# Kernel optimization log

Hardware: AMD Instinct MI355X
Metric: run time of the kernel (lower is better)

Reference implementation:

```python
import jax, jax.numpy as jnp
import numpy as np

D_NODE = 100
D_HID = 300
EPS = 1e-5


def _gru_step_h0(x, W_ih, b_ih, b_hh):
    # Single torch-GRU step with h0 = 0 (seq len 1), so W_hh @ h0 vanishes
    # and only the hidden biases b_hh survive.
    gi = x @ W_ih.T + b_ih                      # [..., 3*H]
    H = D_HID
    r = jax.nn.sigmoid(gi[..., 0:H] + b_hh[0:H])
    z = jax.nn.sigmoid(gi[..., H:2 * H] + b_hh[H:2 * H])
    n = jnp.tanh(gi[..., 2 * H:3 * H] + r * b_hh[2 * H:3 * H])
    return (1.0 - z) * n                        # h' = (1-z)*n + z*0


def setup_inputs() -> dict:
    key = jax.random.key(0)
    ks = jax.random.split(key, 20)
    B, T, Lq, N = 128, 512, 256, 256
    s = 0.02
    inp = {
        "nodes": jax.random.normal(ks[0], (B * N, D_NODE), jnp.float32),
        "context_rep": jax.random.normal(ks[1], (B, Lq, D_HID), jnp.float32),
        "dia_triples": jax.random.randint(ks[2], (B, T, 3), 0, N, jnp.int64 if jax.config.jax_enable_x64 else jnp.int32),
        "node_number": N,
        # mean_trans: Linear(100, 300)
        "W_mean": s * jax.random.normal(ks[3], (D_HID, D_NODE), jnp.float32),
        "b_mean": jnp.zeros((D_HID,), jnp.float32),
        # bidirectional GRU(300 -> 300); h0=0 so W_hh drops out, keep biases
        "W_ih_f": s * jax.random.normal(ks[4], (3 * D_HID, D_HID), jnp.float32),
        "b_ih_f": s * jax.random.normal(ks[5], (3 * D_HID,), jnp.float32),
        "b_hh_f": s * jax.random.normal(ks[6], (3 * D_HID,), jnp.float32),
        "W_ih_b": s * jax.random.normal(ks[7], (3 * D_HID, D_HID), jnp.float32),
        "b_ih_b": s * jax.random.normal(ks[8], (3 * D_HID,), jnp.float32),
        "b_hh_b": s * jax.random.normal(ks[9], (3 * D_HID,), jnp.float32),
        # output_trans: Linear(600, 300) + tanh
        "W_out": s * jax.random.normal(ks[10], (D_HID, 2 * D_HID), jnp.float32),
        "b_out": jnp.zeros((D_HID,), jnp.float32),
        # trans_node_to_decoder_dim: Linear(100, 300)
        "W_node": s * jax.random.normal(ks[11], (D_HID, D_NODE), jnp.float32),
        "b_node": jnp.zeros((D_HID,), jnp.float32),
        # layernorm(300)
        "gamma": jnp.ones((D_HID,), jnp.float32),
        "beta": jnp.zeros((D_HID,), jnp.float32),
    }
    return inp


def reference(nodes, context_rep, dia_triples, node_number,
              W_mean, b_mean, W_ih_f, b_ih_f, b_hh_f,
              W_ih_b, b_ih_b, b_hh_b, W_out, b_out,
              W_node, b_node, gamma, beta):
    B = context_rep.shape[0]
    N = node_number
    T = dia_triples.shape[1]
    nodes3 = nodes.reshape(B, N, D_NODE)                        # per-dialogue node slices

    # gather head/tail nodes of each triple, mean-aggregate
    head = jnp.broadcast_to(dia_triples[:, :, 0][:, :, None], (B, T, D_NODE))
    tail = jnp.broadcast_to(dia_triples[:, :, -1][:, :, None], (B, T, D_NODE))
    gh = jnp.take_along_axis(nodes3, head, axis=1)              # [B,T,100]
    gt = jnp.take_along_axis(nodes3, tail, axis=1)
    tri_mean = 0.5 * (gh + gt)

    x = tri_mean @ W_mean.T + b_mean                            # [B,T,300] GRU inputs (len-1 paths)

    # bidirectional GRU, one step each direction from h0=0
    h_f = _gru_step_h0(x, W_ih_f, b_ih_f, b_hh_f)
    h_b = _gru_step_h0(x, W_ih_b, b_ih_b, b_hh_b)
    hidden = jnp.concatenate([h_f, h_b], axis=-1)               # [B,T,600]

    hid_ = jnp.tanh(hidden @ W_out.T + b_out)                   # [B,T,300]

    # attention: alpha = softmax(query @ hidden^T, -1).sum(0)
    scores = jnp.einsum("bld,btd->blt", context_rep, hid_)
    alpha = jax.nn.softmax(scores, axis=-1).sum(axis=1)         # [B,T]
    rep = jnp.einsum("bt,btd->bd", alpha, hid_)                 # [B,300]

    mu = rep.mean(axis=-1, keepdims=True)
    var = rep.var(axis=-1, keepdims=True)
    path_feature = (rep - mu) * jax.lax.rsqrt(var + EPS) * gamma + beta
    # dropout is identity in eval mode

    node_feature = nodes3 @ W_node.T + b_node                   # [B,N,300]
    node_mask = jnp.zeros((B, 1, N), dtype=bool)                # equal lengths -> no padding
    return path_feature, node_feature, node_mask
```

## Files before the change

### kernel.cpp

```cpp
#include <hip/hip_runtime.h>
#include <math.h>

#define D_NODE 100
#define D_HID  300
static const int TSEQ = 512, LQn = 256, NNODE = 256;

typedef unsigned int u32;
typedef unsigned short u16;
typedef __attribute__((ext_vector_type(8))) short bf16x8;
typedef __attribute__((ext_vector_type(4))) float f32x4;

__device__ __forceinline__ float bflo(u32 u){ return __uint_as_float(u << 16); }
__device__ __forceinline__ float bfhi(u32 u){ return __uint_as_float(u & 0xffff0000u); }
__device__ __forceinline__ float bf2f(u16 v){ return __uint_as_float(((u32)v) << 16); }
__device__ __forceinline__ u16 f2bf(float f){
    u32 u = __float_as_uint(f);
    return (u16)((u + 0x7fffu + ((u >> 16) & 1u)) >> 16);
}
__device__ __forceinline__ u32 pack_bf(float lo, float hi){
    return ((u32)f2bf(lo)) | (((u32)f2bf(hi)) << 16);
}
__device__ __forceinline__ void gload_lds16(const void* g, void* l){
    __builtin_amdgcn_global_load_lds(
        (const __attribute__((address_space(1))) u32*)g,
        (__attribute__((address_space(3))) u32*)l, 16, 0, 0);
}
__device__ __forceinline__ float fsig(float x){
    return __builtin_amdgcn_rcpf(1.f + __expf(-x));
}
__device__ __forceinline__ float ftanh(float x){
    return 1.f - 2.f*__builtin_amdgcn_rcpf(1.f + __expf(2.f*x));
}

__global__ __launch_bounds__(128)
void k0_prep(const float* __restrict__ Wm, const float* __restrict__ bm,
             const float* __restrict__ Wihf, const float* __restrict__ bihf, const float* __restrict__ bhhf,
             const float* __restrict__ Wihb, const float* __restrict__ bihb, const float* __restrict__ bhhb,
             u16* __restrict__ W4bf, float* __restrict__ bc, float* __restrict__ bhhn)
{
    int j = blockIdx.x, g = blockIdx.y, dir = blockIdx.z;
    int tid = threadIdx.x;
    u16* wout = W4bf + ((size_t)((dir*3+g)*320 + j))*128;
    if (j >= D_HID) {
        wout[tid] = 0;
        if (tid == 0) { bc[(dir*3+g)*320 + j] = 0.f; if (g==2) bhhn[dir*320+j] = 0.f; }
        return;
    }
    const float* Wih = dir ? Wihb : Wihf;
    const float* bih = dir ? bihb : bihf;
    const float* bhh = dir ? bhhb : bhhf;
    const float* wrow = Wih + (size_t)(g*D_HID + j)*D_HID;
    int k = tid;
    float s = 0.f;
    if (k < D_NODE)
        for (int q = 0; q < D_HID; ++q)
            s = fmaf(wrow[q], Wm[q*D_NODE + k], s);
    wout[k] = f2bf(k < D_NODE ? s : 0.f);

    __shared__ float red[128];
    float p = 0.f;
    for (int q = tid; q < D_HID; q += 128) p = fmaf(bm[q], wrow[q], p);
    red[tid] = p;
    __syncthreads();
    for (int off = 64; off > 0; off >>= 1) {
        if (tid < off) red[tid] += red[tid + off];
        __syncthreads();
    }
    if (tid == 0) {
        float base = bih[g*D_HID + j] + red[0];
        if (g < 2) base += bhh[g*D_HID + j];
        bc[(dir*3+g)*320 + j] = base;
        if (g == 2) bhhn[dir*320 + j] = bhh[2*D_HID + j];
    }
}

__global__ __launch_bounds__(256)
void kW(const float* __restrict__ Wout, const float* __restrict__ Wnode,
        u16* __restrict__ Woutbf, u16* __restrict__ Wnbf)
{
    int idx = blockIdx.x*256 + threadIdx.x;
    if (idx < 384*608) {
        int j = idx / 608, k = idx % 608;
        float v = (j < D_HID && k < 600) ? Wout[(size_t)j*600 + k] : 0.f;
        Woutbf[idx] = f2bf(v);
    } else {
        int i2 = idx - 384*608;
        if (i2 < 320*128) {
            int j = i2 >> 7, k = i2 & 127;
            float v = (j < D_HID && k < D_NODE) ? Wnode[(size_t)j*D_NODE + k] : 0.f;
            Wnbf[i2] = f2bf(v);
        }
    }
}

__global__ __launch_bounds__(256)
void kA(const float* __restrict__ nodes, const int* __restrict__ trip,
        u32* __restrict__ Abf, u32* __restrict__ Nbf)
{
    int gid = blockIdx.x*256 + threadIdx.x;
    if (gid < 65536) {
        int b = gid >> 9;
        int hidx = trip[(size_t)gid*3];
        int tidx = trip[(size_t)gid*3 + 2];
        const float4* nh = (const float4*)(nodes + ((size_t)b*NNODE + hidx)*D_NODE);
        const float4* nt = (const float4*)(nodes + ((size_t)b*NNODE + tidx)*D_NODE);
        u32* ar = Abf + (size_t)gid*64;
        #pragma unroll 5
        for (int i = 0; i < 25; ++i) {
            float4 a = nh[i], c = nt[i];
            ar[i*2]   = pack_bf(0.5f*(a.x+c.x), 0.5f*(a.y+c.y));
            ar[i*2+1] = pack_bf(0.5f*(a.z+c.z), 0.5f*(a.w+c.w));
        }
        #pragma unroll
        for (int i = 50; i < 64; ++i) ar[i] = 0;
    } else {
        int r = gid - 65536;
        if (r < 32768) {
            const float4* nr = (const float4*)(nodes + (size_t)r*D_NODE);
            u32* ar = Nbf + (size_t)r*64;
            #pragma unroll 5
            for (int i = 0; i < 25; ++i) {
                float4 a = nr[i];
                ar[i*2]   = pack_bf(a.x, a.y);
                ar[i*2+1] = pack_bf(a.z, a.w);
            }
            #pragma unroll
            for (int i = 50; i < 64; ++i) ar[i] = 0;
        }
    }
}

__global__ __launch_bounds__(256)
void kC(const float* __restrict__ ctx, u32* __restrict__ Cbf)
{
    int idx = blockIdx.x*256 + threadIdx.x;
    int r = idx / 160, cp = idx % 160;
    int col = cp*2;
    u32 v = 0;
    if (col < D_HID) {
        float2 f = *(const float2*)(ctx + (size_t)r*D_HID + col);
        v = pack_bf(f.x, f.y);
    }
    Cbf[(size_t)r*160 + cp] = v;
}

__global__ __launch_bounds__(256)
void k1_gru(const u16* __restrict__ Abf, const u16* __restrict__ W4bf,
            const float* __restrict__ bc, const float* __restrict__ bhhn,
            u16* __restrict__ H)
{
    __shared__ char smem[16384];
    int tid = threadIdx.x;
    int lane = tid & 63, w = tid >> 6;
    int l15 = lane & 15, lq = lane >> 4;
    int m0 = blockIdx.x * 64;
    int dir = blockIdx.y / 5;
    int jg = blockIdx.y % 5;
    int j0w = jg*64 + w*16;

    bf16x8 bfr[3][4];
    const u16* Wb = W4bf + (size_t)dir*3*320*128;
    #pragma unroll
    for (int g = 0; g < 3; ++g)
        #pragma unroll
        for (int ks = 0; ks < 4; ++ks)
            bfr[g][ks] = *(const bf16x8*)(Wb + ((size_t)(g*320 + j0w + l15))*128 + ks*32 + lq*8);

    #pragma unroll
    for (int ks = 0; ks < 4; ++ks) {
        const u16* g = Abf + ((size_t)(m0 + w*16 + l15))*128 + ks*32 + lq*8;
        gload_lds16(g, smem + (size_t)((w*4 + ks)*64)*16);
    }
    __syncthreads();

    f32x4 acc[4][3];
    #pragma unroll
    for (int ms = 0; ms < 4; ++ms)
        #pragma unroll
        for (int g = 0; g < 3; ++g)
            acc[ms][g] = (f32x4){0.f,0.f,0.f,0.f};

    #pragma unroll
    for (int ms = 0; ms < 4; ++ms)
        #pragma unroll
        for (int ks = 0; ks < 4; ++ks) {
            bf16x8 a = *(const bf16x8*)(smem + (size_t)(((ms*4+ks)*64 + lane))*16);
            acc[ms][0] = __builtin_amdgcn_mfma_f32_16x16x32_bf16(a, bfr[0][ks], acc[ms][0], 0,0,0);
            acc[ms][1] = __builtin_amdgcn_mfma_f32_16x16x32_bf16(a, bfr[1][ks], acc[ms][1], 0,0,0);
            acc[ms][2] = __builtin_amdgcn_mfma_f32_16x16x32_bf16(a, bfr[2][ks], acc[ms][2], 0,0,0);
        }

    int j = j0w + l15;
    float bcr = bc[(dir*3+0)*320 + j];
    float bcz = bc[(dir*3+1)*320 + j];
    float bcn = bc[(dir*3+2)*320 + j];
    float bn2 = bhhn[dir*320 + j];
    bool ok = (j < D_HID);
    #pragma unroll
    for (int ms = 0; ms < 4; ++ms)
        #pragma unroll
        for (int i = 0; i < 4; ++i) {
            float r = fsig(acc[ms][0][i] + bcr);
            float z = fsig(acc[ms][1][i] + bcz);
            float n = ftanh(acc[ms][2][i] + bcn + r*bn2);
            float h = (1.f - z)*n;
            if (ok) H[(size_t)(m0 + ms*16 + lq*4 + i)*608 + dir*D_HID + j] = f2bf(h);
        }
}

__global__ __launch_bounds__(256, 2)
void k2_out(const u16* __restrict__ H, const u16* __restrict__ Woutbf,
            const float* __restrict__ bout, u16* __restrict__ Hid)
{
    __shared__ char smem[40960];
    int tid = threadIdx.x;
    int lane = tid & 63, w = tid >> 6;
    int l15 = lane & 15, lq = lane >> 4;
    int m0 = blockIdx.x * 64;
    int j0 = blockIdx.y * 128;
    int jA = j0 + w*16, jB = j0 + 64 + w*16;

    bf16x8 bA[19], bB[19];
    #pragma unroll
    for (int ks = 0; ks < 19; ++ks) {
        bA[ks] = *(const bf16x8*)(Woutbf + ((size_t)(jA + l15))*608 + ks*32 + lq*8);
        bB[ks] = *(const bf16x8*)(Woutbf + ((size_t)(jB + l15))*608 + ks*32 + lq*8);
    }
    f32x4 acc[4][2];
    #pragma unroll
    for (int ms = 0; ms < 4; ++ms) { acc[ms][0] = (f32x4){0,0,0,0}; acc[ms][1] = (f32x4){0,0,0,0}; }

    #pragma unroll
    for (int c = 0; c < 2; ++c) {
        const int kb = c ? 10 : 0;
        const int nks = c ? 9 : 10;
        #pragma unroll
        for (int kk = 0; kk < 10; ++kk)
            if (kk < nks) {
                const u16* g = H + ((size_t)(m0 + w*16 + l15))*608 + (kb+kk)*32 + lq*8;
                gload_lds16(g, smem + (size_t)((w*10 + kk)*64)*16);
            }
        __syncthreads();
        #pragma unroll
        for (int ms = 0; ms < 4; ++ms)
            #pragma unroll
            for (int kk = 0; kk < 10; ++kk)
                if (kk < nks) {
                    bf16x8 a = *(const bf16x8*)(smem + (size_t)(((ms*10+kk)*64 + lane))*16);
                    acc[ms][0] = __builtin_amdgcn_mfma_f32_16x16x32_bf16(a, bA[kb+kk], acc[ms][0], 0,0,0);
                    acc[ms][1] = __builtin_amdgcn_mfma_f32_16x16x32_bf16(a, bB[kb+kk], acc[ms][1], 0,0,0);
                }
        __syncthreads();
    }

    #pragma unroll
    for (int jj = 0; jj < 2; ++jj) {
        int j = (jj ? jB : jA) + l15;
        if (j < 320) {
            bool real = (j < D_HID);
            float bo = real ? bout[j] : 0.f;
            #pragma unroll
            for (int ms = 0; ms < 4; ++ms)
                #pragma unroll
                for (int i = 0; i < 4; ++i) {
                    u16 v = real ? f2bf(ftanh(acc[ms][jj][i] + bo)) : (u16)0;
                    Hid[(size_t)(m0 + ms*16 + lq*4 + i)*320 + j] = v;
                }
        }
    }
}

__global__ __launch_bounds__(256, 2)
void k3_attn(const u16* __restrict__ Cbf, const u16* __restrict__ Hid,
             float* __restrict__ alphap)
{
    __shared__ char smemA[4096];
    __shared__ char smemB[32768];
    __shared__ float rmax[64*4], rsum[64*4];
    int tid = threadIdx.x;
    int lane = tid & 63, w = tid >> 6;
    int l15 = lane & 15, lq = lane >> 4;
    int b = blockIdx.y;
    int mblk = blockIdx.x;
    const u16* Ab = Cbf + ((size_t)b*LQn + mblk*64)*320;
    const u16* Bb = Hid + ((size_t)b*TSEQ)*320;

    f32x4 acc[4][8];
    #pragma unroll
    for (int ms = 0; ms < 4; ++ms)
        #pragma unroll
        for (int g = 0; g < 8; ++g)
            acc[ms][g] = (f32x4){0,0,0,0};

    for (int ks = 0; ks < 10; ++ks) {
        gload_lds16(Ab + ((size_t)(w*16 + l15))*320 + ks*32 + lq*8,
                    smemA + (size_t)(w*64)*16);
        #pragma unroll
        for (int i = 0; i < 8; ++i) {
            int nt = w*8 + i;
            gload_lds16(Bb + ((size_t)(nt*16 + l15))*320 + ks*32 + lq*8,
                        smemB + (size_t)(nt*64)*16);
        }
        __syncthreads();
        bf16x8 afr[4];
        #pragma unroll
        for (int ms = 0; ms < 4; ++ms)
            afr[ms] = *(const bf16x8*)(smemA + (size_t)((ms*64 + lane))*16);
        #pragma unroll
        for (int i = 0; i < 8; ++i) {
            bf16x8 bfr = *(const bf16x8*)(smemB + (size_t)(((w*8+i)*64 + lane))*16);
            #pragma unroll
            for (int ms = 0; ms < 4; ++ms)
                acc[ms][i] = __builtin_amdgcn_mfma_f32_16x16x32_bf16(afr[ms], bfr, acc[ms][i], 0,0,0);
        }
        __syncthreads();
    }

    #pragma unroll
    for (int ms = 0; ms < 4; ++ms)
        #pragma unroll
        for (int i = 0; i < 4; ++i) {
            float m = acc[ms][0][i];
            #pragma unroll
            for (int g = 1; g < 8; ++g) m = fmaxf(m, acc[ms][g][i]);
            m = fmaxf(m, __shfl_xor(m, 1));
            m = fmaxf(m, __shfl_xor(m, 2));
            m = fmaxf(m, __shfl_xor(m, 4));
            m = fmaxf(m, __shfl_xor(m, 8));
            if (l15 == 0) rmax[(ms*16 + lq*4 + i)*4 + w] = m;
        }
    __syncthreads();
    float mfin[4][4];
    #pragma unroll
    for (int ms = 0; ms < 4; ++ms)
        #pragma unroll
        for (int i = 0; i < 4; ++i) {
            float4 mv = *(const float4*)&rmax[(ms*16 + lq*4 + i)*4];
            mfin[ms][i] = fmaxf(fmaxf(mv.x, mv.y), fmaxf(mv.z, mv.w));
        }
    #pragma unroll
    for (int ms = 0; ms < 4; ++ms)
        #pragma unroll
        for (int i = 0; i < 4; ++i) {
            float s = 0.f;
            #pragma unroll
            for (int g = 0; g < 8; ++g) {
                float e = __expf(acc[ms][g][i] - mfin[ms][i]);
                acc[ms][g][i] = e;
                s += e;
            }
            s += __shfl_xor(s, 1);
            s += __shfl_xor(s, 2);
            s += __shfl_xor(s, 4);
            s += __shfl_xor(s, 8);
            if (l15 == 0) rsum[(ms*16 + lq*4 + i)*4 + w] = s;
        }
    __syncthreads();
    float inv[4][4];
    #pragma unroll
    for (int ms = 0; ms < 4; ++ms)
        #pragma unroll
        for (int i = 0; i < 4; ++i) {
            float4 sv = *(const float4*)&rsum[(ms*16 + lq*4 + i)*4];
            inv[ms][i] = __builtin_amdgcn_rcpf(sv.x + sv.y + sv.z + sv.w);
        }
    float* ap = alphap + ((size_t)b*4 + mblk)*TSEQ;
    #pragma unroll
    for (int g = 0; g < 8; ++g) {
        float c = 0.f;
        #pragma unroll
        for (int ms = 0; ms < 4; ++ms)
            #pragma unroll
            for (int i = 0; i < 4; ++i)
                c = fmaf(acc[ms][g][i], inv[ms][i], c);
        c += __shfl_xor(c, 16);
        c += __shfl_xor(c, 32);
        if (lq == 0) ap[w*128 + g*16 + l15] = c;
    }
}

__global__ __launch_bounds__(320)
void k4_rep(const float* __restrict__ alphap, const u16* __restrict__ Hid,
            const float* __restrict__ gamma, const float* __restrict__ beta,
            float* __restrict__ outP)
{
    __shared__ float al[512];
    __shared__ float rs[5], rss[5];
    int tid = threadIdx.x, b = blockIdx.x;
    const float* ap = alphap + (size_t)b*4*TSEQ;
    for (int i = tid; i < 512; i += 320)
        al[i] = ap[i] + ap[512 + i] + ap[1024 + i] + ap[1536 + i];
    __syncthreads();
    float acc = 0.f;
    if (tid < D_HID) {
        const u16* hp = Hid + (size_t)b*TSEQ*320 + tid;
        #pragma unroll 8
        for (int t = 0; t < TSEQ; ++t)
            acc = fmaf(al[t], bf2f(hp[(size_t)t*320]), acc);
    }
    float v = (tid < D_HID) ? acc : 0.f;
    float s = v, q = v*v;
    #pragma unroll
    for (int off = 32; off > 0; off >>= 1) { s += __shfl_xor(s, off, 64); q += __shfl_xor(q, off, 64); }
    if ((tid & 63) == 0) { rs[tid >> 6] = s; rss[tid >> 6] = q; }
    __syncthreads();
    float S = rs[0]+rs[1]+rs[2]+rs[3]+rs[4];
    float Q = rss[0]+rss[1]+rss[2]+rss[3]+rss[4];
    float mu = S * (1.f/300.f);
    float var = Q * (1.f/300.f) - mu*mu;
    if (tid < D_HID)
        outP[(size_t)b*D_HID + tid] = (acc - mu) * rsqrtf(var + 1e-5f) * gamma[tid] + beta[tid];
}

__global__ __launch_bounds__(256)
void k5_node(const u16* __restrict__ Nbf, const u16* __restrict__ Wnbf,
             const float* __restrict__ bn, float* __restrict__ outN)
{
    __shared__ char smem[16384];
    int tid = threadIdx.x;
    int lane = tid & 63, w = tid >> 6;
    int l15 = lane & 15, lq = lane >> 4;
    int m0 = blockIdx.x * 64;
    int j0w = blockIdx.y*64 + w*16;

    bf16x8 bw[4];
    #pragma unroll
    for (int ks = 0; ks < 4; ++ks)
        bw[ks] = *(const bf16x8*)(Wnbf + ((size_t)(j0w + l15))*128 + ks*32 + lq*8);

    #pragma unroll
    for (int ks = 0; ks < 4; ++ks) {
        const u16* g = Nbf + ((size_t)(m0 + w*16 + l15))*128 + ks*32 + lq*8;
        gload_lds16(g, smem + (size_t)((w*4 + ks)*64)*16);
    }
    __syncthreads();

    f32x4 acc[4];
    #pragma unroll
    for (int ms = 0; ms < 4; ++ms) acc[ms] = (f32x4){0,0,0,0};
    #pragma unroll
    for (int ms = 0; ms < 4; ++ms)
        #pragma unroll
        for (int ks = 0; ks < 4; ++ks) {
            bf16x8 a = *(const bf16x8*)(smem + (size_t)(((ms*4+ks)*64 + lane))*16);
            acc[ms] = __builtin_amdgcn_mfma_f32_16x16x32_bf16(a, bw[ks], acc[ms], 0,0,0);
        }

    int j = j0w + l15;
    if (j < D_HID) {
        float bo = bn[j];
        #pragma unroll
        for (int ms = 0; ms < 4; ++ms)
            #pragma unroll
            for (int i = 0; i < 4; ++i)
                outN[(size_t)(m0 + ms*16 + lq*4 + i)*D_HID + j] = acc[ms][i] + bo;
    }
}

extern "C" void kernel_launch(void* const* d_in, const int* in_sizes, int n_in,
                              void* d_out, int out_size, void* d_ws, size_t ws_size,
                              hipStream_t stream) {
    const float* nodes  = (const float*)d_in[0];
    const float* ctx    = (const float*)d_in[1];
    const int*   trip   = (const int*)d_in[2];
    const float* Wm     = (const float*)d_in[4];
    const float* bm     = (const float*)d_in[5];
    const float* Wihf   = (const float*)d_in[6];
    const float* bihf   = (const float*)d_in[7];
    const float* bhhf   = (const float*)d_in[8];
    const float* Wihb   = (const float*)d_in[9];
    const float* bihb   = (const float*)d_in[10];
    const float* bhhb   = (const float*)d_in[11];
    const float* Wout   = (const float*)d_in[12];
    const float* bout   = (const float*)d_in[13];
    const float* Wnode  = (const float*)d_in[14];
    const float* bnode  = (const float*)d_in[15];
    const float* gamma  = (const float*)d_in[16];
    const float* beta   = (const float*)d_in[17];
    float* out = (float*)d_out;

    char* ws = (char*)d_ws;
    u16*   W4bf   = (u16*)(ws);
    u16*   Woutbf = (u16*)(ws + 491520);
    u16*   Wnbf   = (u16*)(ws + 958464);
    float* bc     = (float*)(ws + 1040384);
    float* bhhn   = (float*)(ws + 1048064);
    char*  Hbase  = ws + 1050624;
    u16*   H      = (u16*)Hbase;
    u32*   Cbf    = (u32*)(Hbase + 33554432ull);
    char*  hidbase = Hbase + 79691776ull;
    u16*   Hid    = (u16*)hidbase;
    u32*   Abf    = (u32*)hidbase;
    u32*   Nbf    = (u32*)(hidbase + 16777216ull);
    float* alphap = (float*)(ws + 122685440ull);

    k0_prep<<<dim3(320,3,2), 128, 0, stream>>>(Wm,bm,Wihf,bihf,bhhf,Wihb,bihb,bhhb,W4bf,bc,bhhn);
    kW     <<<1072, 256, 0, stream>>>(Wout,Wnode,Woutbf,Wnbf);
    kA     <<<384,  256, 0, stream>>>(nodes,trip,Abf,Nbf);
    k1_gru <<<dim3(1024,10), 256, 0, stream>>>((const u16*)Abf,W4bf,bc,bhhn,H);
    k5_node<<<dim3(512,5),   256, 0, stream>>>((const u16*)Nbf,Wnbf,bnode,out + 38400);
    k2_out <<<dim3(1024,3),  256, 0, stream>>>(H,Woutbf,bout,Hid);
    kC     <<<20480, 256, 0, stream>>>(ctx, Cbf);
    k3_attn<<<dim3(4,128),   256, 0, stream>>>((const u16*)Cbf, Hid, alphap);
    k4_rep <<<128,           320, 0, stream>>>(alphap,Hid,gamma,beta,out);
    hipMemsetAsync(out + 38400 + 9830400, 0, 32768*sizeof(float), stream);
}
```

Before: 442.1 us.

## Fuse prep kernels, widen GRU tile, stage epilogue stores, fold rep into attention

Merges the weight conversion and gather kernels into one launch. The GRU kernel now covers 128 rows per block and stages its outputs through LDS so they can be written with 16-byte vector stores; H is laid out with a 304-column stride per direction, and Wout is padded to match. The output projection epilogue is also staged through LDS for vector stores. The alpha-weighted sum over hidden states moves into the attention kernel, which writes partial rep vectors, leaving k4 with a small reduction plus layernorm. This cuts launches, uncoalesced 2-byte stores, and one extra pass over Hid, at the cost of more LDS and registers in k1.

Measured after the change: 461.7 us. +4.4%, slower.

```diff
diff --git a/kernel.cpp b/kernel.cpp
--- a/kernel.cpp
+++ b/kernel.cpp
@@ -75,47 +75,31 @@
 }
 
 __global__ __launch_bounds__(256)
-void kW(const float* __restrict__ Wout, const float* __restrict__ Wnode,
-        u16* __restrict__ Woutbf, u16* __restrict__ Wnbf)
-{
-    int idx = blockIdx.x*256 + threadIdx.x;
-    if (idx < 384*608) {
-        int j = idx / 608, k = idx % 608;
-        float v = (j < D_HID && k < 600) ? Wout[(size_t)j*600 + k] : 0.f;
-        Woutbf[idx] = f2bf(v);
-    } else {
-        int i2 = idx - 384*608;
-        if (i2 < 320*128) {
-            int j = i2 >> 7, k = i2 & 127;
-            float v = (j < D_HID && k < D_NODE) ? Wnode[(size_t)j*D_NODE + k] : 0.f;
-            Wnbf[i2] = f2bf(v);
-        }
-    }
-}
-
-__global__ __launch_bounds__(256)
-void kA(const float* __restrict__ nodes, const int* __restrict__ trip,
-        u32* __restrict__ Abf, u32* __restrict__ Nbf)
-{
-    int gid = blockIdx.x*256 + threadIdx.x;
-    if (gid < 65536) {
-        int b = gid >> 9;
-        int hidx = trip[(size_t)gid*3];
-        int tidx = trip[(size_t)gid*3 + 2];
-        const float4* nh = (const float4*)(nodes + ((size_t)b*NNODE + hidx)*D_NODE);
-        const float4* nt = (const float4*)(nodes + ((size_t)b*NNODE + tidx)*D_NODE);
-        u32* ar = Abf + (size_t)gid*64;
-        #pragma unroll 5
-        for (int i = 0; i < 25; ++i) {
-            float4 a = nh[i], c = nt[i];
-            ar[i*2]   = pack_bf(0.5f*(a.x+c.x), 0.5f*(a.y+c.y));
-            ar[i*2+1] = pack_bf(0.5f*(a.z+c.z), 0.5f*(a.w+c.w));
-        }
-        #pragma unroll
-        for (int i = 50; i < 64; ++i) ar[i] = 0;
-    } else {
-        int r = gid - 65536;
-        if (r < 32768) {
+void kAW(const float* __restrict__ nodes, const int* __restrict__ trip,
+         const float* __restrict__ Wout, const float* __restrict__ Wnode,
+         u32* __restrict__ Abf, u32* __restrict__ Nbf,
+         u16* __restrict__ Woutbf, u16* __restrict__ Wnbf)
+{
+    int blk = blockIdx.x;
+    if (blk < 384) {
+        int gid = blk*256 + threadIdx.x;
+        if (gid < 65536) {
+            int b = gid >> 9;
+            int hidx = trip[(size_t)gid*3];
+            int tidx = trip[(size_t)gid*3 + 2];
+            const float4* nh = (const float4*)(nodes + ((size_t)b*NNODE + hidx)*D_NODE);
+            const float4* nt = (const float4*)(nodes + ((size_t)b*NNODE + tidx)*D_NODE);
+            u32* ar = Abf + (size_t)gid*64;
+            #pragma unroll 5
+            for (int i = 0; i < 25; ++i) {
+                float4 a = nh[i], c = nt[i];
+                ar[i*2]   = pack_bf(0.5f*(a.x+c.x), 0.5f*(a.y+c.y));
+                ar[i*2+1] = pack_bf(0.5f*(a.z+c.z), 0.5f*(a.w+c.w));
+            }
+            #pragma unroll
+            for (int i = 50; i < 64; ++i) ar[i] = 0;
+        } else {
+            int r = gid - 65536;
             const float4* nr = (const float4*)(nodes + (size_t)r*D_NODE);
             u32* ar = Nbf + (size_t)r*64;
             #pragma unroll 5
@@ -127,6 +111,21 @@
             #pragma unroll
             for (int i = 50; i < 64; ++i) ar[i] = 0;
         }
+    } else {
+        int idx = (blk - 384)*256 + threadIdx.x;
+        if (idx < 384*608) {
+            int j = idx / 608, k = idx % 608;
+            int d = k / 304, jj = k - d*304;
+            float v = (j < D_HID && jj < D_HID) ? Wout[(size_t)j*600 + d*D_HID + jj] : 0.f;
+            Woutbf[idx] = f2bf(v);
+        } else {
+            int i2 = idx - 384*608;
+            if (i2 < 320*128) {
+                int j = i2 >> 7, k = i2 & 127;
+                float v = (j < D_HID && k < D_NODE) ? Wnode[(size_t)j*D_NODE + k] : 0.f;
+                Wnbf[i2] = f2bf(v);
+            }
+        }
     }
 }
 
@@ -144,16 +143,16 @@
     Cbf[(size_t)r*160 + cp] = v;
 }
 
-__global__ __launch_bounds__(256)
+__global__ __launch_bounds__(256, 2)
 void k1_gru(const u16* __restrict__ Abf, const u16* __restrict__ W4bf,
             const float* __restrict__ bc, const float* __restrict__ bhhn,
             u16* __restrict__ H)
 {
-    __shared__ char smem[16384];
+    __shared__ char smem[32768];
     int tid = threadIdx.x;
     int lane = tid & 63, w = tid >> 6;
     int l15 = lane & 15, lq = lane >> 4;
-    int m0 = blockIdx.x * 64;
+    int m0 = blockIdx.x * 128;
     int dir = blockIdx.y / 5;
     int jg = blockIdx.y % 5;
     int j0w = jg*64 + w*16;
@@ -167,21 +166,24 @@
             bfr[g][ks] = *(const bf16x8*)(Wb + ((size_t)(g*320 + j0w + l15))*128 + ks*32 + lq*8);
 
     #pragma unroll
-    for (int ks = 0; ks < 4; ++ks) {
-        const u16* g = Abf + ((size_t)(m0 + w*16 + l15))*128 + ks*32 + lq*8;
-        gload_lds16(g, smem + (size_t)((w*4 + ks)*64)*16);
-    }
-    __syncthreads();
-
-    f32x4 acc[4][3];
-    #pragma unroll
-    for (int ms = 0; ms < 4; ++ms)
+    for (int mi = 0; mi < 2; ++mi) {
+        int ms = w + mi*4;
+        #pragma unroll
+        for (int ks = 0; ks < 4; ++ks)
+            gload_lds16(Abf + ((size_t)(m0 + ms*16 + l15))*128 + ks*32 + lq*8,
+                        smem + (size_t)((ms*4 + ks)*64)*16);
+    }
+    __syncthreads();
+
+    f32x4 acc[8][3];
+    #pragma unroll
+    for (int ms = 0; ms < 8; ++ms)
         #pragma unroll
         for (int g = 0; g < 3; ++g)
             acc[ms][g] = (f32x4){0.f,0.f,0.f,0.f};
 
     #pragma unroll
-    for (int ms = 0; ms < 4; ++ms)
+    for (int ms = 0; ms < 8; ++ms)
         #pragma unroll
         for (int ks = 0; ks < 4; ++ks) {
             bf16x8 a = *(const bf16x8*)(smem + (size_t)(((ms*4+ks)*64 + lane))*16);
@@ -195,17 +197,30 @@
     float bcz = bc[(dir*3+1)*320 + j];
     float bcn = bc[(dir*3+2)*320 + j];
     float bn2 = bhhn[dir*320 + j];
-    bool ok = (j < D_HID);
-    #pragma unroll
-    for (int ms = 0; ms < 4; ++ms)
+
+    __syncthreads();
+    u16* lt = (u16*)smem + w*128*24;
+    #pragma unroll
+    for (int ms = 0; ms < 8; ++ms)
         #pragma unroll
         for (int i = 0; i < 4; ++i) {
             float r = fsig(acc[ms][0][i] + bcr);
             float z = fsig(acc[ms][1][i] + bcz);
             float n = ftanh(acc[ms][2][i] + bcn + r*bn2);
             float h = (1.f - z)*n;
-            if (ok) H[(size_t)(m0 + ms*16 + lq*4 + i)*608 + dir*D_HID + j] = f2bf(h);
-        }
+            lt[(ms*16 + lq*4 + i)*24 + l15] = f2bf(h);
+        }
+    if (j0w < 304) {
+        #pragma unroll
+        for (int half = 0; half < 2; ++half) {
+            int r = half*64 + lane;
+            uint4 v0 = *(const uint4*)(lt + r*24);
+            uint4 v1 = *(const uint4*)(lt + r*24 + 8);
+            u16* dst = H + (size_t)(m0 + r)*608 + dir*304 + j0w;
+            *(uint4*)dst = v0;
+            *(uint4*)(dst + 8) = v1;
+        }
+    }
 }
 
 __global__ __launch_bounds__(256, 2)
@@ -253,30 +268,38 @@
         __syncthreads();
     }
 
+    u16* lt = (u16*)smem + w*64*24;
     #pragma unroll
     for (int jj = 0; jj < 2; ++jj) {
-        int j = (jj ? jB : jA) + l15;
-        if (j < 320) {
-            bool real = (j < D_HID);
-            float bo = real ? bout[j] : 0.f;
-            #pragma unroll
-            for (int ms = 0; ms < 4; ++ms)
-                #pragma unroll
-                for (int i = 0; i < 4; ++i) {
-                    u16 v = real ? f2bf(ftanh(acc[ms][jj][i] + bo)) : (u16)0;
-                    Hid[(size_t)(m0 + ms*16 + lq*4 + i)*320 + j] = v;
-                }
-        }
+        int jX = jj ? jB : jA;
+        if (jX >= 320) continue;
+        int j = jX + l15;
+        bool real = (j < D_HID);
+        float bo = real ? bout[j] : 0.f;
+        #pragma unroll
+        for (int ms = 0; ms < 4; ++ms)
+            #pragma unroll
+            for (int i = 0; i < 4; ++i) {
+                float v = real ? ftanh(acc[ms][jj][i] + bo) : 0.f;
+                lt[(ms*16 + lq*4 + i)*24 + l15] = f2bf(v);
+            }
+        int r = lane;
+        uint4 v0 = *(const uint4*)(lt + r*24);
+        uint4 v1 = *(const uint4*)(lt + r*24 + 8);
+        u16* dst = Hid + (size_t)(m0 + r)*320 + jX;
+        *(uint4*)dst = v0;
+        *(uint4*)(dst + 8) = v1;
     }
 }
 
 __global__ __launch_bounds__(256, 2)
 void k3_attn(const u16* __restrict__ Cbf, const u16* __restrict__ Hid,
-             float* __restrict__ alphap)
+             float* __restrict__ repp)
 {
     __shared__ char smemA[4096];
     __shared__ char smemB[32768];
     __shared__ float rmax[64*4], rsum[64*4];
+    __shared__ float csa[512];
     int tid = threadIdx.x;
     int lane = tid & 63, w = tid >> 6;
     int l15 = lane & 15, lq = lane >> 4;
@@ -364,7 +387,6 @@
             float4 sv = *(const float4*)&rsum[(ms*16 + lq*4 + i)*4];
             inv[ms][i] = __builtin_amdgcn_rcpf(sv.x + sv.y + sv.z + sv.w);
         }
-    float* ap = alphap + ((size_t)b*4 + mblk)*TSEQ;
     #pragma unroll
     for (int g = 0; g < 8; ++g) {
         float c = 0.f;
@@ -375,29 +397,31 @@
                 c = fmaf(acc[ms][g][i], inv[ms][i], c);
         c += __shfl_xor(c, 16);
         c += __shfl_xor(c, 32);
-        if (lq == 0) ap[w*128 + g*16 + l15] = c;
+        if (lq == 0) csa[w*128 + g*16 + l15] = c;
+    }
+    __syncthreads();
+    float* rp = repp + ((size_t)b*4 + mblk)*320;
+    for (int j = tid; j < 320; j += 256) {
+        const u16* hp = Bb + j;
+        float a = 0.f;
+        #pragma unroll 8
+        for (int t = 0; t < TSEQ; ++t)
+            a = fmaf(csa[t], bf2f(hp[(size_t)t*320]), a);
+        rp[j] = a;
     }
 }
 
 __global__ __launch_bounds__(320)
-void k4_rep(const float* __restrict__ alphap, const u16* __restrict__ Hid,
+void k4_rep(const float* __restrict__ repp,
             const float* __restrict__ gamma, const float* __restrict__ beta,
             float* __restrict__ outP)
 {
-    __shared__ float al[512];
     __shared__ float rs[5], rss[5];
     int tid = threadIdx.x, b = blockIdx.x;
-    const float* ap = alphap + (size_t)b*4*TSEQ;
-    for (int i = tid; i < 512; i += 320)
-        al[i] = ap[i] + ap[512 + i] + ap[1024 + i] + ap[1536 + i];
-    __syncthreads();
+    const float* rp = repp + (size_t)b*4*320;
     float acc = 0.f;
-    if (tid < D_HID) {
-        const u16* hp = Hid + (size_t)b*TSEQ*320 + tid;
-        #pragma unroll 8
-        for (int t = 0; t < TSEQ; ++t)
-            acc = fmaf(al[t], bf2f(hp[(size_t)t*320]), acc);
-    }
+    if (tid < D_HID)
+        acc = rp[tid] + rp[320 + tid] + rp[640 + tid] + rp[960 + tid];
     float v = (tid < D_HID) ? acc : 0.f;
     float s = v, q = v*v;
     #pragma unroll
@@ -492,16 +516,15 @@
     u16*   Hid    = (u16*)hidbase;
     u32*   Abf    = (u32*)hidbase;
     u32*   Nbf    = (u32*)(hidbase + 16777216ull);
-    float* alphap = (float*)(ws + 122685440ull);
+    float* repp   = (float*)(ws + 122685440ull);
 
     k0_prep<<<dim3(320,3,2), 128, 0, stream>>>(Wm,bm,Wihf,bihf,bhhf,Wihb,bihb,bhhb,W4bf,bc,bhhn);
-    kW     <<<1072, 256, 0, stream>>>(Wout,Wnode,Woutbf,Wnbf);
-    kA     <<<384,  256, 0, stream>>>(nodes,trip,Abf,Nbf);
-    k1_gru <<<dim3(1024,10), 256, 0, stream>>>((const u16*)Abf,W4bf,bc,bhhn,H);
+    kAW    <<<1456, 256, 0, stream>>>(nodes,trip,Wout,Wnode,Abf,Nbf,Woutbf,Wnbf);
+    k1_gru <<<dim3(512,10),  256, 0, stream>>>((const u16*)Abf,W4bf,bc,bhhn,H);
     k5_node<<<dim3(512,5),   256, 0, stream>>>((const u16*)Nbf,Wnbf,bnode,out + 38400);
     k2_out <<<dim3(1024,3),  256, 0, stream>>>(H,Woutbf,bout,Hid);
     kC     <<<20480, 256, 0, stream>>>(ctx, Cbf);
-    k3_attn<<<dim3(4,128),   256, 0, stream>>>((const u16*)Cbf, Hid, alphap);
-    k4_rep <<<128,           320, 0, stream>>>(alphap,Hid,gamma,beta,out);
+    k3_attn<<<dim3(4,128),   256, 0, stream>>>((const u16*)Cbf, Hid, repp);
+    k4_rep <<<128,           320, 0, stream>>>(repp,gamma,beta,out);
     hipMemsetAsync(out + 38400 + 9830400, 0, 32768*sizeof(float), stream);
 }
```
